# Kernel tuning notes

Hardware: AMD Instinct MI355X
Metric: run time of the kernel (lower is better)

Reference implementation:

```python
import jax, jax.numpy as jnp
import numpy as np

N_NODES = 50000
N_EDGES = 800000
F_IN = 24
H = 128
N_GRAPHS = 100
BN_EPS = 1e-5


def setup_inputs() -> dict:
    key = jax.random.key(0)
    ks = jax.random.split(key, 12)
    x = jax.random.normal(ks[0], (N_NODES, F_IN), dtype=jnp.float32)
    edge_index = jax.random.randint(ks[1], (2, N_EDGES), 0, N_NODES, dtype=jnp.int32)
    batch = (jnp.arange(N_NODES, dtype=jnp.int32) // (N_NODES // N_GRAPHS)).astype(jnp.int32)

    def lin(k, fan_in, fan_out):
        bound = 1.0 / np.sqrt(fan_in)
        kw, kb = jax.random.split(k)
        W = jax.random.uniform(kw, (fan_in, fan_out), jnp.float32, -bound, bound)
        b = jax.random.uniform(kb, (fan_out,), jnp.float32, -bound, bound)
        return W, b

    W1, b1 = lin(ks[2], 2 * F_IN, H)
    W2, b2 = lin(ks[3], 2 * H, H)
    W3, b3 = lin(ks[4], 2 * H, H)
    Wl, bl = lin(ks[5], H, 1)
    g1 = jnp.ones((H,), jnp.float32); be1 = jnp.zeros((H,), jnp.float32)
    g2 = jnp.ones((H,), jnp.float32); be2 = jnp.zeros((H,), jnp.float32)
    g3 = jnp.ones((H,), jnp.float32); be3 = jnp.zeros((H,), jnp.float32)
    return {"x": x, "edge_index": edge_index, "batch": batch,
            "W1": W1, "b1": b1, "W2": W2, "b2": b2, "W3": W3, "b3": b3,
            "g1": g1, "be1": be1, "g2": g2, "be2": be2, "g3": g3, "be3": be3,
            "Wl": Wl, "bl": bl}


def edge_conv(x, src, dst, W, b):
    # PyG EdgeConv: message = mlp([x_i, x_j - x_i]) for edge j->i, aggr=max at i
    x_i = x[dst]                                    # [E, F]
    e = jnp.concatenate([x_i, x[src] - x_i], axis=-1)  # [E, 2F]
    m = jax.nn.relu(e @ W + b)                      # [E, H]
    out = jax.ops.segment_max(m, dst, num_segments=N_NODES)
    return jnp.where(jnp.isfinite(out), out, 0.0)   # isolated nodes -> 0


def batch_norm(h, g, b):
    # training-mode BN over node dim (biased variance), dropout treated as identity
    mu = h.mean(axis=0)
    var = ((h - mu) ** 2).mean(axis=0)
    return g * (h - mu) * jax.lax.rsqrt(var + BN_EPS) + b


def reference(x, edge_index, batch, W1, b1, W2, b2, W3, b3,
              g1, be1, g2, be2, g3, be3, Wl, bl):
    src, dst = edge_index[0], edge_index[1]
    h = edge_conv(x, src, dst, W1, b1)
    h = jax.nn.relu(batch_norm(h, g1, be1))
    h = edge_conv(h, src, dst, W2, b2)
    h = jax.nn.relu(batch_norm(h, g2, be2))
    h = edge_conv(h, src, dst, W3, b3)
    h = batch_norm(h, g3, be3)
    # global_mean_pool
    sums = jax.ops.segment_sum(h, batch, num_segments=N_GRAPHS)           # [G, H]
    counts = jax.ops.segment_sum(jnp.ones((h.shape[0],), h.dtype), batch,
                                 num_segments=N_GRAPHS)
    pooled = sums / jnp.maximum(counts, 1.0)[:, None]
    return jax.nn.relu(pooled @ Wl + bl)                                  # [G, 1]
```

## Files before the change

kernel.cpp:

```cpp
#include <hip/hip_runtime.h>

#define N_NODES 50000
#define N_EDGES 800000
#define F_IN 24
#define HDIM 128
#define N_GRAPHS 100
#define BN_EPS 1e-5f
#define NBLK 196
#define ROWS_PER_GRAPH (N_NODES / N_GRAPHS)
#define MM_GRID 782
#define HIST_BLKS ((N_EDGES + 255) / 256)
#define PREP_BLKS (F_IN + 2 * HDIM)
#define SSTR 32
#define SUMS_PER_LAYER (256 * SSTR)
#define STATS_BLKS 392
#define POOL_CHUNKS 10
#define POOL_BLKS (N_GRAPHS * POOL_CHUNKS)
#define ROWS_PER_CHUNK (ROWS_PER_GRAPH / POOL_CHUNKS)


typedef _Float16 h2 __attribute__((ext_vector_type(2)));
typedef _Float16 h4 __attribute__((ext_vector_type(4)));
typedef _Float16 f16x8 __attribute__((ext_vector_type(8)));
typedef float f32x4 __attribute__((ext_vector_type(4)));

template <int K, int KC>
__global__ __launch_bounds__(256) void k_mm1(const float* __restrict__ X,
                                             const float* __restrict__ Wcat,
                                             const float* __restrict__ bias,
                                             _Float16* __restrict__ A, _Float16* __restrict__ C) {
    __shared__ float Xs[KC * 68];
    __shared__ float Ws[KC * 256];
    int tid = threadIdx.x;
    int row0 = blockIdx.x * 64;
    int cg = tid & 31;
    int rg = tid >> 5;

    float accA[8][4], accC[8][4];
#pragma unroll
    for (int ri = 0; ri < 8; ++ri)
#pragma unroll
        for (int ci = 0; ci < 4; ++ci) {
            accA[ri][ci] = bias[cg * 4 + ci];
            accC[ri][ci] = 0.f;
        }

    for (int k0 = 0; k0 < K; k0 += KC) {
        __syncthreads();
        {
            const int C4 = KC / 4;
            for (int i = tid; i < 64 * C4; i += 256) {
                int c4 = i % C4, r = i / C4;
                int row = row0 + r;
                float4 v = make_float4(0.f, 0.f, 0.f, 0.f);
                if (row < N_NODES) v = *(const float4*)&X[row * K + k0 + c4 * 4];
                Xs[(c4 * 4 + 0) * 68 + r] = v.x;
                Xs[(c4 * 4 + 1) * 68 + r] = v.y;
                Xs[(c4 * 4 + 2) * 68 + r] = v.z;
                Xs[(c4 * 4 + 3) * 68 + r] = v.w;
            }
        }
        for (int i = tid; i < KC * 64; i += 256) {
            int c4 = i & 63, kr = i >> 6;
            *(float4*)&Ws[kr * 256 + c4 * 4] =
                *(const float4*)&Wcat[(k0 + kr) * 256 + c4 * 4];
        }
        __syncthreads();
#pragma unroll
        for (int kk = 0; kk < KC; ++kk) {
            float4 t0 = *(const float4*)&Xs[kk * 68 + rg * 8];
            float4 t1 = *(const float4*)&Xs[kk * 68 + rg * 8 + 4];
            float4 wa = *(const float4*)&Ws[kk * 256 + cg * 4];
            float4 wc = *(const float4*)&Ws[kk * 256 + 128 + cg * 4];
            float t[8] = {t0.x, t0.y, t0.z, t0.w, t1.x, t1.y, t1.z, t1.w};
            float wav[4] = {wa.x, wa.y, wa.z, wa.w};
            float wcv[4] = {wc.x, wc.y, wc.z, wc.w};
#pragma unroll
            for (int ri = 0; ri < 8; ++ri)
#pragma unroll
                for (int ci = 0; ci < 4; ++ci) {
                    accA[ri][ci] += t[ri] * wav[ci];
                    accC[ri][ci] += t[ri] * wcv[ci];
                }
        }
    }

#pragma unroll
    for (int ri = 0; ri < 8; ++ri) {
        int row = row0 + rg * 8 + ri;
        if (row < N_NODES) {
            union { h2 h[2]; uint2 u; } pa;
            pa.h[0] = h2{(_Float16)accA[ri][0], (_Float16)accA[ri][1]};
            pa.h[1] = h2{(_Float16)accA[ri][2], (_Float16)accA[ri][3]};
            *(uint2*)&A[row * HDIM + cg * 4] = pa.u;
            union { h2 h[2]; uint2 u; } pk;
            pk.h[0] = h2{(_Float16)accC[ri][0], (_Float16)accC[ri][1]};
            pk.h[1] = h2{(_Float16)accC[ri][2], (_Float16)accC[ri][3]};
            *(uint2*)&C[row * HDIM + cg * 4] = pk.u;
        }
    }
}

__global__ __launch_bounds__(256) void k_mmf(const _Float16* __restrict__ X,
                                             const _Float16* __restrict__ Wf,
                                             const float* __restrict__ bias,
                                             const float* __restrict__ sums,
                                             const float* __restrict__ g,
                                             const float* __restrict__ be,
                                             _Float16* __restrict__ A, _Float16* __restrict__ C) {
    __shared__ _Float16 Xh[16 * 520];
    __shared__ _Float16 Wh[128 * 128];
    __shared__ float scs[128], shs[128];
    int tid = threadIdx.x;
    int lane = tid & 63, wv = tid >> 6;
    int row0 = blockIdx.x * 64;

    if (tid < 128) {
        float S  = sums[tid * SSTR];
        float S2 = sums[(128 + tid) * SSTR];
        float mean = S / (float)N_NODES;
        float var = fmaxf(S2 / (float)N_NODES - mean * mean, 0.f);
        float scv = g[tid] / sqrtf(var + BN_EPS);
        scs[tid] = scv;
        shs[tid] = be[tid] - mean * scv;
    }
    {
        const uint4* s = (const uint4*)Wf;
        uint4* d = (uint4*)Wh;
        for (int i = tid; i < 2048; i += 256) d[i] = s[i];
    }
    __syncthreads();
    for (int i = tid; i < 64 * 32; i += 256) {
        int k4 = i & 31, rl = i >> 5;
        int row = row0 + rl;
        float4 v = make_float4(0.f, 0.f, 0.f, 0.f);
        if (row < N_NODES) {
            h4 xv = *(const h4*)&X[row * HDIM + k4 * 4];
            v = make_float4((float)xv.x, (float)xv.y, (float)xv.z, (float)xv.w);
        }
        int c = k4 * 4;
        v.x = fmaxf(v.x * scs[c + 0] + shs[c + 0], 0.f);
        v.y = fmaxf(v.y * scs[c + 1] + shs[c + 1], 0.f);
        v.z = fmaxf(v.z * scs[c + 2] + shs[c + 2], 0.f);
        v.w = fmaxf(v.w * scs[c + 3] + shs[c + 3], 0.f);
        int rt = rl >> 4, m = rl & 15, kc = k4 >> 3, q = (k4 >> 1) & 3, jh = k4 & 1;
        _Float16* dp = Xh + (rt * 4 + kc) * 520 + (q * 16 + m) * 8 + jh * 4;
        dp[0] = (_Float16)v.x; dp[1] = (_Float16)v.y;
        dp[2] = (_Float16)v.z; dp[3] = (_Float16)v.w;
    }
    __syncthreads();

    int n = lane & 15, q = lane >> 4;
    f32x4 acc[8];

#pragma unroll
    for (int nt = 0; nt < 8; ++nt) {
        float b0 = bias[nt * 16 + n];
        acc[nt] = f32x4{b0, b0, b0, b0};
    }
#pragma unroll
    for (int kc = 0; kc < 4; ++kc) {
        f16x8 a = *(const f16x8*)(Xh + (wv * 4 + kc) * 520 + lane * 8);
#pragma unroll
        for (int nt = 0; nt < 8; ++nt) {
            f16x8 b = *(const f16x8*)(Wh + ((nt * 4 + kc) * 64 + lane) * 8);
            acc[nt] = __builtin_amdgcn_mfma_f32_16x16x32_f16(a, b, acc[nt], 0, 0, 0);
        }
    }
#pragma unroll
    for (int nt = 0; nt < 8; ++nt) {
#pragma unroll
        for (int r = 0; r < 4; ++r) {
            int row = row0 + wv * 16 + q * 4 + r;
            if (row < N_NODES) A[row * HDIM + nt * 16 + n] = (_Float16)acc[nt][r];
        }
    }
    __syncthreads();
    {
        const uint4* s = (const uint4*)(Wf + 16384);
        uint4* d = (uint4*)Wh;
        for (int i = tid; i < 2048; i += 256) d[i] = s[i];
    }
    __syncthreads();

#pragma unroll
    for (int nt = 0; nt < 8; ++nt) acc[nt] = f32x4{0.f, 0.f, 0.f, 0.f};
#pragma unroll
    for (int kc = 0; kc < 4; ++kc) {
        f16x8 a = *(const f16x8*)(Xh + (wv * 4 + kc) * 520 + lane * 8);
#pragma unroll
        for (int nt = 0; nt < 8; ++nt) {
            f16x8 b = *(const f16x8*)(Wh + ((nt * 4 + kc) * 64 + lane) * 8);
            acc[nt] = __builtin_amdgcn_mfma_f32_16x16x32_f16(a, b, acc[nt], 0, 0, 0);
        }
    }
#pragma unroll
    for (int nt = 0; nt < 8; ++nt) {
#pragma unroll
        for (int r = 0; r < 4; ++r) {
            int row = row0 + wv * 16 + q * 4 + r;
            if (row < N_NODES) C[row * HDIM + nt * 16 + n] = (_Float16)acc[nt][r];
        }
    }
}

__global__ void k_pre(const float* __restrict__ W1, const float* __restrict__ W2,
                      const float* __restrict__ W3, float* __restrict__ Wcat1,
                      _Float16* __restrict__ Wf2, _Float16* __restrict__ Wf3,
                      const int* __restrict__ dst, unsigned* __restrict__ deg,
                      unsigned* __restrict__ rank) {
    int b = blockIdx.x;
    int j = threadIdx.x;
    if (b < F_IN) {
        float wb = W1[(b + F_IN) * HDIM + (j & 127)];
        float wt = W1[b * HDIM + (j & 127)];
        Wcat1[b * 256 + j] = (j < HDIM) ? (wt - wb) : wb;
    } else if (b < PREP_BLKS) {
        int idx = b - F_IN;
        int layer = idx >> 7;
        int k = idx & 127;
        const float* W = layer ? W3 : W2;
        _Float16* Wf   = layer ? Wf3 : Wf2;
        int col = j & 127;
        float wt = W[k * HDIM + col];
        float wb = W[(k + HDIM) * HDIM + col];
        float v = (j < 128) ? (wt - wb) : wb;
        int plane = j >> 7;
        int nt = col >> 4, n = col & 15, kc = k >> 5, q = (k >> 3) & 3, jj = k & 7;
        int f = ((nt * 4 + kc) * 4 + q) * 128 + n * 8 + jj;
        Wf[plane * 16384 + f] = (_Float16)v;
    } else {
        int e = (b - PREP_BLKS) * 256 + j;
        if (e < N_EDGES) rank[e] = atomicAdd(&deg[dst[e]], 1u);
    }
}

__global__ __launch_bounds__(256) void k_scanall(const unsigned* __restrict__ deg,
                                                 unsigned* __restrict__ bsum,
                                                 unsigned* __restrict__ off) {
    __shared__ unsigned s[256];
    int t = threadIdx.x;
    int b = blockIdx.x;
    int i = b * 256 + t;
    unsigned v = (i < N_NODES) ? deg[i] : 0u;
    s[t] = v;
    __syncthreads();
    for (int d = 1; d < 256; d <<= 1) {
        unsigned u = (t >= d) ? s[t - d] : 0u;
        __syncthreads();
        s[t] += u;
        __syncthreads();
    }
    unsigned locex = s[t] - v;
    if (t == 255) atomicExch(&bsum[b], s[255] + 1u);
    __syncthreads();
    unsigned bs = 0;
    if (t < NBLK) {
        unsigned x;
        do { x = atomicAdd(&bsum[t], 0u); } while (x == 0u);
        bs = x - 1u;
    }
    s[t] = (t < NBLK) ? bs : 0u;
    __syncthreads();
    for (int d = 1; d < 256; d <<= 1) {
        unsigned u = (t >= d) ? s[t - d] : 0u;
        __syncthreads();
        s[t] += u;
        __syncthreads();
    }
    unsigned bexcl = (b == 0) ? 0u : s[b - 1];
    if (i < N_NODES) off[i] = bexcl + locex;
}

__global__ void k_scatter(const int* __restrict__ src, const int* __restrict__ dst,
                          const unsigned* __restrict__ off, const unsigned* __restrict__ rank,
                          unsigned* __restrict__ ssrc) {
    int e = blockIdx.x * 256 + threadIdx.x;
    if (e < N_EDGES)
        ssrc[off[dst[e]] + rank[e]] = (unsigned)src[e];
}

__global__ __launch_bounds__(256) void k_agg(const h2* __restrict__ A,
                                             const h2* __restrict__ Cc,
                                             const unsigned* __restrict__ off,
                                             const unsigned* __restrict__ deg,
                                             const unsigned* __restrict__ ssrc,
                                             h2* __restrict__ H) {
    __shared__ unsigned sl[4][64];
    int w = threadIdx.x >> 6;
    int lane = threadIdx.x & 63;
    int i = blockIdx.x * 4 + w;
    int d = (int)deg[i];
    unsigned o = off[i];
    h2 a = A[i * 64 + lane];
    union { unsigned short us[2]; h2 v; } ninf;
    ninf.us[0] = 0xFC00; ninf.us[1] = 0xFC00;
    const h2 NI = ninf.v;
    h2 m2 = NI;
    for (int base = 0; base < d; base += 64) {
        int cntc = min(64, d - base);
        if (lane < cntc) sl[w][lane] = ssrc[o + base + lane];
        int e = 0;
        for (; e + 16 <= cntc; e += 16) {
            unsigned s[16];
#pragma unroll
            for (int j = 0; j < 16; ++j) s[j] = sl[w][e + j];
            h2 v[16];
#pragma unroll
            for (int j = 0; j < 16; ++j) v[j] = Cc[s[j] * 64 + lane];
#pragma unroll
            for (int st = 8; st > 0; st >>= 1)
#pragma unroll
                for (int j = 0; j < st; ++j)
                    v[j] = __builtin_elementwise_max(v[j], v[j + st]);
            m2 = __builtin_elementwise_max(m2, v[0]);
        }
        if (e + 8 <= cntc) {
            unsigned s[8];
#pragma unroll
            for (int j = 0; j < 8; ++j) s[j] = sl[w][e + j];
            h2 v[8];
#pragma unroll
            for (int j = 0; j < 8; ++j) v[j] = Cc[s[j] * 64 + lane];
#pragma unroll
            for (int st = 4; st > 0; st >>= 1)
#pragma unroll
                for (int j = 0; j < st; ++j)
                    v[j] = __builtin_elementwise_max(v[j], v[j + st]);
            m2 = __builtin_elementwise_max(m2, v[0]);
            e += 8;
        }
        if (e < cntc) {
            int last = cntc - 1;
            unsigned s[8];
#pragma unroll
            for (int j = 0; j < 8; ++j) {
                int idx = e + j;
                s[j] = sl[w][idx < last ? idx : last];
            }
            h2 v[8];
#pragma unroll
            for (int j = 0; j < 8; ++j) v[j] = Cc[s[j] * 64 + lane];
#pragma unroll
            for (int j = 0; j < 8; ++j)
                if (e + j >= cntc) v[j] = NI;
#pragma unroll
            for (int st = 4; st > 0; st >>= 1)
#pragma unroll
                for (int j = 0; j < st; ++j)
                    v[j] = __builtin_elementwise_max(v[j], v[j + st]);
            m2 = __builtin_elementwise_max(m2, v[0]);
        }
    }
    float hx = (d > 0) ? fmaxf((float)a.x + (float)m2.x, 0.f) : 0.f;
    float hy = (d > 0) ? fmaxf((float)a.y + (float)m2.y, 0.f) : 0.f;
    H[i * 64 + lane] = h2{(_Float16)hx, (_Float16)hy};
}

__global__ __launch_bounds__(256) void k_stats(const _Float16* __restrict__ H,
                                               float* __restrict__ sums) {
    __shared__ float4 ls[256], ls2[256];
    int t = threadIdx.x;
    int c4 = t & 31, rg = t >> 5;
    int row0 = blockIdx.x * 128;
    float4 s = make_float4(0.f, 0.f, 0.f, 0.f);
    float4 s2 = make_float4(0.f, 0.f, 0.f, 0.f);
#pragma unroll 4
    for (int it = 0; it < 16; ++it) {
        int row = row0 + rg * 16 + it;
        if (row < N_NODES) {
            h4 hv = *(const h4*)&H[row * HDIM + c4 * 4];
            float4 v = make_float4((float)hv.x, (float)hv.y, (float)hv.z, (float)hv.w);
            s.x += v.x; s.y += v.y; s.z += v.z; s.w += v.w;
            s2.x += v.x * v.x; s2.y += v.y * v.y; s2.z += v.z * v.z; s2.w += v.w * v.w;
        }
    }
    ls[t] = s; ls2[t] = s2;
    __syncthreads();
    if (t < 32) {
        float4 a = ls[t], a2 = ls2[t];
#pragma unroll
        for (int j = 1; j < 8; ++j) {
            float4 b = ls[j * 32 + t], b2 = ls2[j * 32 + t];
            a.x += b.x; a.y += b.y; a.z += b.z; a.w += b.w;
            a2.x += b2.x; a2.y += b2.y; a2.z += b2.z; a2.w += b2.w;
        }
        int c = t * 4;
        atomicAdd(&sums[(c + 0) * SSTR], a.x);
        atomicAdd(&sums[(c + 1) * SSTR], a.y);
        atomicAdd(&sums[(c + 2) * SSTR], a.z);
        atomicAdd(&sums[(c + 3) * SSTR], a.w);
        atomicAdd(&sums[(128 + c + 0) * SSTR], a2.x);
        atomicAdd(&sums[(128 + c + 1) * SSTR], a2.y);
        atomicAdd(&sums[(128 + c + 2) * SSTR], a2.z);
        atomicAdd(&sums[(128 + c + 3) * SSTR], a2.w);
    }
}

__global__ __launch_bounds__(256) void k_pool2(const _Float16* __restrict__ H,
                                               float* __restrict__ Pp,
                                               float* __restrict__ sums) {
    __shared__ float4 ls[256], ls2[256];
    int t = threadIdx.x;
    int c4 = t & 31, rg = t >> 5;
    int b = blockIdx.x;
    int base = (b / POOL_CHUNKS) * ROWS_PER_GRAPH + (b % POOL_CHUNKS) * ROWS_PER_CHUNK;
    float4 s = make_float4(0.f, 0.f, 0.f, 0.f);
    float4 s2 = make_float4(0.f, 0.f, 0.f, 0.f);
#pragma unroll
    for (int j = 0; j < 7; ++j) {
        int rl = rg + j * 8;
        if (rl < ROWS_PER_CHUNK) {
            int row = base + rl;
            h4 hv = *(const h4*)&H[row * HDIM + c4 * 4];
            float4 v = make_float4((float)hv.x, (float)hv.y, (float)hv.z, (float)hv.w);
            s.x += v.x; s.y += v.y; s.z += v.z; s.w += v.w;
            s2.x += v.x * v.x; s2.y += v.y * v.y; s2.z += v.z * v.z; s2.w += v.w * v.w;
        }
    }
    ls[t] = s; ls2[t] = s2;
    __syncthreads();
    if (t < 32) {
        float4 a = ls[t], a2 = ls2[t];
#pragma unroll
        for (int j = 1; j < 8; ++j) {
            float4 q = ls[j * 32 + t], q2 = ls2[j * 32 + t];
            a.x += q.x; a.y += q.y; a.z += q.z; a.w += q.w;
            a2.x += q2.x; a2.y += q2.y; a2.z += q2.z; a2.w += q2.w;
        }
        int c = t * 4;
        *(float4*)&Pp[b * HDIM + c] = a;
        atomicAdd(&sums[(c + 0) * SSTR], a.x);
        atomicAdd(&sums[(c + 1) * SSTR], a.y);
        atomicAdd(&sums[(c + 2) * SSTR], a.z);
        atomicAdd(&sums[(c + 3) * SSTR], a.w);
        atomicAdd(&sums[(128 + c + 0) * SSTR], a2.x);
        atomicAdd(&sums[(128 + c + 1) * SSTR], a2.y);
        atomicAdd(&sums[(128 + c + 2) * SSTR], a2.z);
        atomicAdd(&sums[(128 + c + 3) * SSTR], a2.w);
    }
}

__global__ __launch_bounds__(128) void k_out(const float* __restrict__ Pp,
                                             const float* __restrict__ sums,
                                             const float* __restrict__ g3,
                                             const float* __restrict__ be3,
                                             const float* __restrict__ Wl,
                                             const float* __restrict__ bl,
                                             float* __restrict__ out) {
    int g = blockIdx.x;
    int k = threadIdx.x;
    float S  = sums[k * SSTR];
    float S2 = sums[(128 + k) * SSTR];
    float mean = S / (float)N_NODES;
    float var = fmaxf(S2 / (float)N_NODES - mean * mean, 0.f);
    float scv = g3[k] / sqrtf(var + BN_EPS);
    float shv = be3[k] - mean * scv;
    float pooled = 0.f;
#pragma unroll
    for (int j = 0; j < POOL_CHUNKS; ++j)
        pooled += Pp[(g * POOL_CHUNKS + j) * HDIM + k];
    float p = (scv * (pooled * (1.f / (float)ROWS_PER_GRAPH)) + shv) * Wl[k];
    __shared__ float red[2];
    for (int o = 32; o > 0; o >>= 1) p += __shfl_down(p, o);
    if ((k & 63) == 0) red[k >> 6] = p;
    __syncthreads();
    if (k == 0) out[g] = fmaxf(red[0] + red[1] + bl[0], 0.f);
}

extern "C" void kernel_launch(void* const* d_in, const int* in_sizes, int n_in,
                              void* d_out, int out_size, void* d_ws, size_t ws_size,
                              hipStream_t stream) {
    const float* x   = (const float*)d_in[0];
    const int* ei    = (const int*)d_in[1];
    const float* W1  = (const float*)d_in[3];
    const float* b1  = (const float*)d_in[4];
    const float* W2  = (const float*)d_in[5];
    const float* b2  = (const float*)d_in[6];
    const float* W3  = (const float*)d_in[7];
    const float* b3  = (const float*)d_in[8];
    const float* g1  = (const float*)d_in[9];
    const float* be1 = (const float*)d_in[10];
    const float* g2  = (const float*)d_in[11];
    const float* be2 = (const float*)d_in[12];
    const float* g3  = (const float*)d_in[13];
    const float* be3 = (const float*)d_in[14];
    const float* Wl  = (const float*)d_in[15];
    const float* bl  = (const float*)d_in[16];
    float* out = (float*)d_out;

    const int* srcp = ei;
    const int* dstp = ei + N_EDGES;

    char* ws = (char*)d_ws;
    size_t o = 0;
    auto alloc = [&](size_t bytes) -> void* {
        o = (o + 255) & ~(size_t)255;
        void* p = ws + o;
        o += bytes;
        return p;
    };
    _Float16* A   = (_Float16*)alloc((size_t)N_NODES * HDIM * 2);
    _Float16* C   = (_Float16*)alloc((size_t)N_NODES * HDIM * 2);
    _Float16* h   = (_Float16*)alloc((size_t)N_NODES * HDIM * 2);
    float* Wcat1  = (float*)alloc((size_t)F_IN * 256 * 4);
    _Float16* Wf2 = (_Float16*)alloc((size_t)2 * 16384 * 2);
    _Float16* Wf3 = (_Float16*)alloc((size_t)2 * 16384 * 2);
    unsigned* deg  = (unsigned*)alloc((size_t)N_NODES * 4);
    unsigned* bsum = (unsigned*)alloc((size_t)NBLK * 4);
    float* sums    = (float*)alloc((size_t)3 * SUMS_PER_LAYER * 4);
    unsigned* off  = (unsigned*)alloc((size_t)N_NODES * 4);
    unsigned* rank = (unsigned*)alloc((size_t)N_EDGES * 4);
    unsigned* ssrc = (unsigned*)alloc((size_t)N_EDGES * 4);
    float* Pp      = (float*)alloc((size_t)POOL_BLKS * HDIM * 4);
    (void)ws_size; (void)n_in; (void)in_sizes; (void)out_size;

    float* sums0 = sums;
    float* sums1 = sums + SUMS_PER_LAYER;
    float* sums2 = sums + 2 * SUMS_PER_LAYER;

    size_t zlen = (size_t)((char*)(sums + 3 * SUMS_PER_LAYER) - (char*)deg);
    (void)hipMemsetAsync(deg, 0, zlen, stream);

    k_pre<<<PREP_BLKS + HIST_BLKS, 256, 0, stream>>>(W1, W2, W3, Wcat1, Wf2, Wf3,
                                                     dstp, deg, rank);
    k_scanall<<<NBLK, 256, 0, stream>>>(deg, bsum, off);
    k_scatter<<<HIST_BLKS, 256, 0, stream>>>(srcp, dstp, off, rank, ssrc);

    const int AGB = N_NODES / 4;

    k_mm1<F_IN, F_IN><<<MM_GRID, 256, 0, stream>>>(x, Wcat1, b1, A, C);
    k_agg<<<AGB, 256, 0, stream>>>((const h2*)A, (const h2*)C, off, deg, ssrc, (h2*)h);
    k_stats<<<STATS_BLKS, 256, 0, stream>>>(h, sums0);

    k_mmf<<<MM_GRID, 256, 0, stream>>>(h, Wf2, b2, sums0, g1, be1, A, C);
    k_agg<<<AGB, 256, 0, stream>>>((const h2*)A, (const h2*)C, off, deg, ssrc, (h2*)h);
    k_stats<<<STATS_BLKS, 256, 0, stream>>>(h, sums1);

    k_mmf<<<MM_GRID, 256, 0, stream>>>(h, Wf3, b3, sums1, g2, be2, A, C);
    k_agg<<<AGB, 256, 0, stream>>>((const h2*)A, (const h2*)C, off, deg, ssrc, (h2*)h);

    k_pool2<<<POOL_BLKS, 256, 0, stream>>>(h, Pp, sums2);
    k_out<<<N_GRAPHS, 128, 0, stream>>>(Pp, sums2, g3, be3, Wl, bl, out);
}
```

Measured before the change: 353.3 us.

## Split wavefront across edges with h4 gathers in agg; fuse scatter into mm1

The aggregation kernel now has each half-wavefront gather 8-byte h4 rows for alternating edges, so one wave processes two edges per load instruction. The two partial maxima are combined with a cross-half shuffle before the ReLU and store. Separately, the CSR scatter kernel is folded into the first matmul launch as extra blocks, removing one kernel launch. The agg change halves the lane count per row, which may increase tail waste for low-degree nodes.

```diff
diff --git a/kernel.cpp b/kernel.cpp
--- a/kernel.cpp
+++ b/kernel.cpp
@@ -24,13 +24,33 @@
 typedef _Float16 f16x8 __attribute__((ext_vector_type(8)));
 typedef float f32x4 __attribute__((ext_vector_type(4)));
 
+__device__ inline h4 max4(h4 a, h4 b) { return __builtin_elementwise_max(a, b); }
+__device__ inline h4 shfl_xor_h4(h4 v, int m) {
+    union { h4 h; int2 i; } u;
+    u.h = v;
+    u.i.x = __shfl_xor(u.i.x, m);
+    u.i.y = __shfl_xor(u.i.y, m);
+    return u.h;
+}
+
 template <int K, int KC>
 __global__ __launch_bounds__(256) void k_mm1(const float* __restrict__ X,
                                              const float* __restrict__ Wcat,
                                              const float* __restrict__ bias,
-                                             _Float16* __restrict__ A, _Float16* __restrict__ C) {
+                                             _Float16* __restrict__ A, _Float16* __restrict__ C,
+                                             const int* __restrict__ src,
+                                             const int* __restrict__ dst,
+                                             const unsigned* __restrict__ off,
+                                             const unsigned* __restrict__ rank,
+                                             unsigned* __restrict__ ssrc) {
     __shared__ float Xs[KC * 68];
     __shared__ float Ws[KC * 256];
+    if (blockIdx.x >= MM_GRID) {
+        int e = (blockIdx.x - MM_GRID) * 256 + threadIdx.x;
+        if (e < N_EDGES)
+            ssrc[off[dst[e]] + rank[e]] = (unsigned)src[e];
+        return;
+    }
     int tid = threadIdx.x;
     int row0 = blockIdx.x * 64;
     int cg = tid & 31;
@@ -272,89 +292,73 @@
     if (i < N_NODES) off[i] = bexcl + locex;
 }
 
-__global__ void k_scatter(const int* __restrict__ src, const int* __restrict__ dst,
-                          const unsigned* __restrict__ off, const unsigned* __restrict__ rank,
-                          unsigned* __restrict__ ssrc) {
-    int e = blockIdx.x * 256 + threadIdx.x;
-    if (e < N_EDGES)
-        ssrc[off[dst[e]] + rank[e]] = (unsigned)src[e];
-}
-
-__global__ __launch_bounds__(256) void k_agg(const h2* __restrict__ A,
-                                             const h2* __restrict__ Cc,
+__global__ __launch_bounds__(256) void k_agg(const h4* __restrict__ A,
+                                             const h4* __restrict__ Cc,
                                              const unsigned* __restrict__ off,
                                              const unsigned* __restrict__ deg,
                                              const unsigned* __restrict__ ssrc,
-                                             h2* __restrict__ H) {
+                                             h4* __restrict__ H) {
     __shared__ unsigned sl[4][64];
     int w = threadIdx.x >> 6;
     int lane = threadIdx.x & 63;
     int i = blockIdx.x * 4 + w;
     int d = (int)deg[i];
     unsigned o = off[i];
-    h2 a = A[i * 64 + lane];
-    union { unsigned short us[2]; h2 v; } ninf;
-    ninf.us[0] = 0xFC00; ninf.us[1] = 0xFC00;
-    const h2 NI = ninf.v;
-    h2 m2 = NI;
+    int half = lane >> 5;
+    int cl = lane & 31;
+    h4 a = A[i * 32 + cl];
+    union { unsigned short us[4]; h4 v; } nif;
+    nif.us[0] = 0xFC00; nif.us[1] = 0xFC00; nif.us[2] = 0xFC00; nif.us[3] = 0xFC00;
+    const h4 NI = nif.v;
+    h4 m = NI;
     for (int base = 0; base < d; base += 64) {
-        int cntc = min(64, d - base);
-        if (lane < cntc) sl[w][lane] = ssrc[o + base + lane];
+        int cnt = min(64, d - base);
+        if (lane < cnt) sl[w][lane] = ssrc[o + base + lane];
         int e = 0;
-        for (; e + 16 <= cntc; e += 16) {
-            unsigned s[16];
-#pragma unroll
-            for (int j = 0; j < 16; ++j) s[j] = sl[w][e + j];
-            h2 v[16];
-#pragma unroll
-            for (int j = 0; j < 16; ++j) v[j] = Cc[s[j] * 64 + lane];
-#pragma unroll
-            for (int st = 8; st > 0; st >>= 1)
-#pragma unroll
-                for (int j = 0; j < st; ++j)
-                    v[j] = __builtin_elementwise_max(v[j], v[j + st]);
-            m2 = __builtin_elementwise_max(m2, v[0]);
-        }
-        if (e + 8 <= cntc) {
+        for (; e + 16 <= cnt; e += 16) {
             unsigned s[8];
 #pragma unroll
-            for (int j = 0; j < 8; ++j) s[j] = sl[w][e + j];
-            h2 v[8];
-#pragma unroll
-            for (int j = 0; j < 8; ++j) v[j] = Cc[s[j] * 64 + lane];
+            for (int j = 0; j < 8; ++j) s[j] = sl[w][e + 2 * j + half];
+            h4 v[8];
+#pragma unroll
+            for (int j = 0; j < 8; ++j) v[j] = Cc[s[j] * 32 + cl];
 #pragma unroll
             for (int st = 4; st > 0; st >>= 1)
 #pragma unroll
-                for (int j = 0; j < st; ++j)
-                    v[j] = __builtin_elementwise_max(v[j], v[j + st]);
-            m2 = __builtin_elementwise_max(m2, v[0]);
-            e += 8;
-        }
-        if (e < cntc) {
-            int last = cntc - 1;
+                for (int j = 0; j < st; ++j) v[j] = max4(v[j], v[j + st]);
+            m = max4(m, v[0]);
+        }
+        if (e < cnt) {
+            int last = cnt - 1;
             unsigned s[8];
 #pragma unroll
             for (int j = 0; j < 8; ++j) {
-                int idx = e + j;
+                int idx = e + 2 * j + half;
                 s[j] = sl[w][idx < last ? idx : last];
             }
-            h2 v[8];
-#pragma unroll
-            for (int j = 0; j < 8; ++j) v[j] = Cc[s[j] * 64 + lane];
-#pragma unroll
-            for (int j = 0; j < 8; ++j)
-                if (e + j >= cntc) v[j] = NI;
+            h4 v[8];
+#pragma unroll
+            for (int j = 0; j < 8; ++j) v[j] = Cc[s[j] * 32 + cl];
+#pragma unroll
+            for (int j = 0; j < 8; ++j) {
+                int idx = e + 2 * j + half;
+                if (idx >= cnt) v[j] = NI;
+            }
 #pragma unroll
             for (int st = 4; st > 0; st >>= 1)
 #pragma unroll
-                for (int j = 0; j < st; ++j)
-                    v[j] = __builtin_elementwise_max(v[j], v[j + st]);
-            m2 = __builtin_elementwise_max(m2, v[0]);
-        }
-    }
-    float hx = (d > 0) ? fmaxf((float)a.x + (float)m2.x, 0.f) : 0.f;
-    float hy = (d > 0) ? fmaxf((float)a.y + (float)m2.y, 0.f) : 0.f;
-    H[i * 64 + lane] = h2{(_Float16)hx, (_Float16)hy};
+                for (int j = 0; j < st; ++j) v[j] = max4(v[j], v[j + st]);
+            m = max4(m, v[0]);
+        }
+    }
+    m = max4(m, shfl_xor_h4(m, 32));
+    if (lane < 32) {
+        float h0 = (d > 0) ? fmaxf((float)a.x + (float)m.x, 0.f) : 0.f;
+        float h1 = (d > 0) ? fmaxf((float)a.y + (float)m.y, 0.f) : 0.f;
+        float h2v = (d > 0) ? fmaxf((float)a.z + (float)m.z, 0.f) : 0.f;
+        float h3 = (d > 0) ? fmaxf((float)a.w + (float)m.w, 0.f) : 0.f;
+        H[i * 32 + cl] = h4{(_Float16)h0, (_Float16)h1, (_Float16)h2v, (_Float16)h3};
+    }
 }
 
 __global__ __launch_bounds__(256) void k_stats(const _Float16* __restrict__ H,
@@ -525,20 +529,20 @@
     k_pre<<<PREP_BLKS + HIST_BLKS, 256, 0, stream>>>(W1, W2, W3, Wcat1, Wf2, Wf3,
                                                      dstp, deg, rank);
     k_scanall<<<NBLK, 256, 0, stream>>>(deg, bsum, off);
-    k_scatter<<<HIST_BLKS, 256, 0, stream>>>(srcp, dstp, off, rank, ssrc);
 
     const int AGB = N_NODES / 4;
 
-    k_mm1<F_IN, F_IN><<<MM_GRID, 256, 0, stream>>>(x, Wcat1, b1, A, C);
-    k_agg<<<AGB, 256, 0, stream>>>((const h2*)A, (const h2*)C, off, deg, ssrc, (h2*)h);
+    k_mm1<F_IN, F_IN><<<MM_GRID + HIST_BLKS, 256, 0, stream>>>(
+        x, Wcat1, b1, A, C, srcp, dstp, off, rank, ssrc);
+    k_agg<<<AGB, 256, 0, stream>>>((const h4*)A, (const h4*)C, off, deg, ssrc, (h4*)h);
     k_stats<<<STATS_BLKS, 256, 0, stream>>>(h, sums0);
 
     k_mmf<<<MM_GRID, 256, 0, stream>>>(h, Wf2, b2, sums0, g1, be1, A, C);
-    k_agg<<<AGB, 256, 0, stream>>>((const h2*)A, (const h2*)C, off, deg, ssrc, (h2*)h);
+    k_agg<<<AGB, 256, 0, stream>>>((const h4*)A, (const h4*)C, off, deg, ssrc, (h4*)h);
     k_stats<<<STATS_BLKS, 256, 0, stream>>>(h, sums1);
 
     k_mmf<<<MM_GRID, 256, 0, stream>>>(h, Wf3, b3, sums1, g2, be2, A, C);
-    k_agg<<<AGB, 256, 0, stream>>>((const h2*)A, (const h2*)C, off, deg, ssrc, (h2*)h);
+    k_agg<<<AGB, 256, 0, stream>>>((const h4*)A, (const h4*)C, off, deg, ssrc, (h4*)h);
 
     k_pool2<<<POOL_BLKS, 256, 0, stream>>>(h, Pp, sums2);
     k_out<<<N_GRAPHS, 128, 0, stream>>>(Pp, sums2, g3, be3, Wl, bl, out);
```

After: 355.3 us. No clear change (+0.6%).
